# Kernel optimization log

Measured on AMD Instinct MI355X. Metric: run time of the kernel, lower is better.

## Reference

```python
import jax, jax.numpy as jnp
import numpy as np

B, LQ, LK = 4, 2048, 2048
DIM = 1024          # intermediate_dim
H, D = 16, 64       # num_heads, head_dim
AD = H * D          # attn_dim
SCALE = 1.0 / np.sqrt(D).astype(np.float32)


def setup_inputs() -> dict:
    key = jax.random.key(0)
    ks = jax.random.split(key, 12)
    init = lambda k, shape, fan_in: jax.random.normal(k, shape, jnp.float32) / np.sqrt(fan_in).astype(np.float32)
    return {
        "x": jax.random.normal(ks[0], (B, LQ, DIM), jnp.float32),
        "embeds": jax.random.normal(ks[1], (B, LK, DIM), jnp.float32),
        "Wq": init(ks[2], (DIM, AD), DIM), "bq": jnp.zeros((AD,), jnp.float32),
        "Wk": init(ks[3], (DIM, AD), DIM), "bk": jnp.zeros((AD,), jnp.float32),
        "Wv": init(ks[4], (DIM, AD), DIM), "bv": jnp.zeros((AD,), jnp.float32),
        "Wo": init(ks[5], (AD, DIM), AD), "bo": jnp.zeros((DIM,), jnp.float32),
    }


def reference(x, embeds, Wq, bq, Wk, bk, Wv, bv, Wo, bo):
    b, lq, _ = x.shape
    lk = embeds.shape[1]
    # separate QKV projections (cross-attention: K,V from embeds)
    q = (x @ Wq + bq).reshape(b, lq, H, D)
    k = (embeds @ Wk + bk).reshape(b, lk, H, D)
    v = (embeds @ Wv + bv).reshape(b, lk, H, D)
    # scaled dot-product attention; full [b,h,lq,lk] score matrix (as in source)
    scores = jnp.einsum("bqhd,bkhd->bhqk", q, k) * SCALE
    attn = jax.nn.softmax(scores, axis=-1)  # dropout is identity at eval
    ctx = jnp.einsum("bhqk,bkhd->bqhd", attn, v).reshape(b, lq, AD)
    return ctx @ Wo + bo
```

## Files before the change

kernel.cpp:

```cpp
#include <hip/hip_runtime.h>
#include <cstdint>
#include <cstddef>

#define NB   4
#define NLQ  2048
#define NLK  2048
#define NDIM 1024
#define NH   16
#define ND   64
#define NAD  1024

typedef __attribute__((ext_vector_type(8))) short bf16x8;
typedef __attribute__((ext_vector_type(4))) short sh4;
typedef __attribute__((ext_vector_type(4))) float f32x4;
typedef __attribute__((ext_vector_type(4))) int   i32x4;

static __device__ __forceinline__ short f2bf(float f) {
    unsigned u = __builtin_bit_cast(unsigned, f);
    u += 0x7fffu + ((u >> 16) & 1u);
    return (short)(u >> 16);
}

#define GLL16(GP, LP) __builtin_amdgcn_global_load_lds( \
    (const __attribute__((address_space(1))) void*)(GP), \
    (__attribute__((address_space(3))) void*)(LP), 16, 0, 0)

#define SYNC_LDS do { \
    __builtin_amdgcn_sched_barrier(0); \
    asm volatile("s_waitcnt lgkmcnt(0)" ::: "memory"); \
    __builtin_amdgcn_s_barrier(); \
    asm volatile("" ::: "memory"); \
    __builtin_amdgcn_sched_barrier(0); } while (0)

__global__ void cvt2(const float* __restrict__ x, const float* __restrict__ e,
                     short* __restrict__ xo, short* __restrict__ eo) {
    const float* in = blockIdx.y ? e : x;
    short* out = blockIdx.y ? eo : xo;
    int i = (blockIdx.x * blockDim.x + threadIdx.x) * 4;
    const float4 v = *(const float4*)(in + i);
    sh4 o;
    o.x = f2bf(v.x); o.y = f2bf(v.y); o.z = f2bf(v.z); o.w = f2bf(v.w);
    *(sh4*)(out + i) = o;
}

__global__ void wtrans4(const float* __restrict__ W0, const float* __restrict__ W1,
                        const float* __restrict__ W2, const float* __restrict__ W3,
                        short* __restrict__ T0, short* __restrict__ T1,
                        short* __restrict__ T2, short* __restrict__ T3) {
    __shared__ float t[32][33];
    const int z = blockIdx.z;
    const float* W = (z == 0) ? W0 : (z == 1) ? W1 : (z == 2) ? W2 : W3;
    short* Wt = (z == 0) ? T0 : (z == 1) ? T1 : (z == 2) ? T2 : T3;
    const int bx = blockIdx.x * 32;
    const int by = blockIdx.y * 32;
    const int tx = threadIdx.x & 31, ty = threadIdx.x >> 5;
    #pragma unroll
    for (int i = 0; i < 32; i += 8)
        t[ty + i][tx] = W[(size_t)(bx + ty + i) * 1024 + by + tx];
    __syncthreads();
    #pragma unroll
    for (int i = 0; i < 32; i += 8)
        Wt[(size_t)(by + ty + i) * 1024 + bx + tx] = f2bf(t[tx][ty + i]);
}

static __device__ __forceinline__ void xcd_tile_remap(int f, int& bx, int& by) {
    bx = ((f & 7) << 3) | ((f >> 3) & 7);
    by = f >> 6;
}


__global__ __launch_bounds__(256) void gemm_qkv(const short* __restrict__ Xb,
                                                const short* __restrict__ Eb,
                                                const short* __restrict__ Wqt,
                                                const short* __restrict__ Wkt,
                                                const short* __restrict__ Wvt,
                                                const float* __restrict__ bq,
                                                const float* __restrict__ bk,
                                                const float* __restrict__ bv,
                                                short* __restrict__ Qb,
                                                short* __restrict__ Kf,
                                                short* __restrict__ Vtb)
{
    const int N = 1024, K = 1024;
    __shared__ __align__(16) short As[128 * 64];
    __shared__ __align__(16) short Bs[128 * 64];
    const int z = blockIdx.z;
    const short* A    = (z == 0) ? Xb : Eb;
    const short* Wt   = (z == 0) ? Wqt : (z == 1) ? Wkt : Wvt;
    const float* bias = (z == 0) ? bq : (z == 1) ? bk : bv;
    const float scale = (z == 0) ? 0.18033688011112042f : 1.0f;

    const int tid = threadIdx.x, wave = tid >> 6, lane = tid & 63;
    const int quad = lane >> 4, col = lane & 15;
    int bx, by;
    xcd_tile_remap(blockIdx.x + (blockIdx.y << 6), bx, by);
    const int m0 = bx * 128, n0 = by * 128;
    const int wm = wave >> 1, wn = wave & 1;

    const f32x4 zero = {0.f, 0.f, 0.f, 0.f};
    f32x4 acc[4][4];
    #pragma unroll
    for (int i = 0; i < 4; ++i)
        #pragma unroll
        for (int j = 0; j < 4; ++j)
            acc[i][j] = zero;

    for (int kt = 0; kt < K / 64; ++kt) {
        __syncthreads();
        #pragma unroll
        for (int i = 0; i < 4; ++i) {
            const int f = (i * 4 + wave) * 512 + lane * 8;
            const int row = f >> 6, ch = (f >> 3) & 7;
            const int gcol = kt * 64 + ((ch ^ (row & 7)) * 8);
            GLL16(A  + (size_t)(m0 + row) * K + gcol, &As[f]);
            GLL16(Wt + (size_t)(n0 + row) * K + gcol, &Bs[f]);
        }
        __syncthreads();
        #pragma unroll
        for (int kk = 0; kk < 2; ++kk) {
            bf16x8 af[4], bfr[4];
            #pragma unroll
            for (int mt = 0; mt < 4; ++mt) {
                const int r = wm * 64 + mt * 16 + col;
                af[mt] = *(const bf16x8*)&As[r * 64 + (((kk * 4 + quad) ^ (r & 7)) * 8)];
            }
            #pragma unroll
            for (int nt = 0; nt < 4; ++nt) {
                const int r = wn * 64 + nt * 16 + col;
                bfr[nt] = *(const bf16x8*)&Bs[r * 64 + (((kk * 4 + quad) ^ (r & 7)) * 8)];
            }
            #pragma unroll
            for (int mt = 0; mt < 4; ++mt)
                #pragma unroll
                for (int nt = 0; nt < 4; ++nt)
                    acc[mt][nt] = __builtin_amdgcn_mfma_f32_16x16x32_bf16(af[mt], bfr[nt], acc[mt][nt], 0, 0, 0);
        }
    }

    if (z < 2) {
        short* outp = (z == 0) ? Qb : Kf;
        #pragma unroll
        for (int mt = 0; mt < 4; ++mt)
            #pragma unroll
            for (int nt = 0; nt < 4; ++nt) {
                const int n = n0 + wn * 64 + nt * 16 + col;
                const float bv_ = bias[n];
                #pragma unroll
                for (int r = 0; r < 4; ++r) {
                    const int m = m0 + wm * 64 + mt * 16 + quad * 4 + r;
                    outp[(size_t)m * N + n] = f2bf((acc[mt][nt][r] + bv_) * scale);
                }
            }
    } else {
        #pragma unroll
        for (int mt = 0; mt < 4; ++mt)
            #pragma unroll
            for (int nt = 0; nt < 4; ++nt) {
                const int n = n0 + wn * 64 + nt * 16 + col;
                const int hh = n >> 6, d = n & 63;
                const float bv_ = bias[n];
                const int mb = m0 + wm * 64 + mt * 16 + quad * 4;
                const int bb = mb >> 11, s = mb & 2047;
                sh4 o4;
                #pragma unroll
                for (int r = 0; r < 4; ++r)
                    o4[r] = f2bf(acc[mt][nt][r] + bv_);
                *(sh4*)&Vtb[((size_t)((bb * NH + hh) * 64 + d)) * NLK + s] = o4;
            }
    }
}

__global__ __launch_bounds__(256) void gemm_out(const short* __restrict__ A,
                                                const short* __restrict__ Wt,
                                                const float* __restrict__ bias,
                                                float* __restrict__ outp)
{
    const int N = 1024, K = 1024;
    __shared__ __align__(16) short As[128 * 64];
    __shared__ __align__(16) short Bs[128 * 64];
    const int tid = threadIdx.x, wave = tid >> 6, lane = tid & 63;
    const int quad = lane >> 4, col = lane & 15;
    int bx, by;
    xcd_tile_remap(blockIdx.x + (blockIdx.y << 6), bx, by);
    const int m0 = bx * 128, n0 = by * 128;
    const int wm = wave >> 1, wn = wave & 1;

    const f32x4 zero = {0.f, 0.f, 0.f, 0.f};
    f32x4 acc[4][4];
    #pragma unroll
    for (int i = 0; i < 4; ++i)
        #pragma unroll
        for (int j = 0; j < 4; ++j)
            acc[i][j] = zero;

    for (int kt = 0; kt < K / 64; ++kt) {
        __syncthreads();
        #pragma unroll
        for (int i = 0; i < 4; ++i) {
            const int f = (i * 4 + wave) * 512 + lane * 8;
            const int row = f >> 6, ch = (f >> 3) & 7;
            const int gcol = kt * 64 + ((ch ^ (row & 7)) * 8);
            GLL16(A  + (size_t)(m0 + row) * K + gcol, &As[f]);
            GLL16(Wt + (size_t)(n0 + row) * K + gcol, &Bs[f]);
        }
        __syncthreads();
        #pragma unroll
        for (int kk = 0; kk < 2; ++kk) {
            bf16x8 af[4], bfr[4];
            #pragma unroll
            for (int mt = 0; mt < 4; ++mt) {
                const int r = wm * 64 + mt * 16 + col;
                af[mt] = *(const bf16x8*)&As[r * 64 + (((kk * 4 + quad) ^ (r & 7)) * 8)];
            }
            #pragma unroll
            for (int nt = 0; nt < 4; ++nt) {
                const int r = wn * 64 + nt * 16 + col;
                bfr[nt] = *(const bf16x8*)&Bs[r * 64 + (((kk * 4 + quad) ^ (r & 7)) * 8)];
            }
            #pragma unroll
            for (int mt = 0; mt < 4; ++mt)
                #pragma unroll
                for (int nt = 0; nt < 4; ++nt)
                    acc[mt][nt] = __builtin_amdgcn_mfma_f32_16x16x32_bf16(af[mt], bfr[nt], acc[mt][nt], 0, 0, 0);
        }
    }

    #pragma unroll
    for (int mt = 0; mt < 4; ++mt)
        #pragma unroll
        for (int nt = 0; nt < 4; ++nt) {
            const int n = n0 + wn * 64 + nt * 16 + col;
            const float bv_ = bias[n];
            #pragma unroll
            for (int r = 0; r < 4; ++r) {
                const int m = m0 + wm * 64 + mt * 16 + quad * 4 + r;
                outp[(size_t)m * N + n] = acc[mt][nt][r] + bv_;
            }
        }
}

__global__ __launch_bounds__(256, 2) void attn_fused9(const short* __restrict__ Q,
                                                      const short* __restrict__ Kb,
                                                      const short* __restrict__ Vt,
                                                      short* __restrict__ ctx)
{
    __shared__ __align__(16) short Ks[2][64 * 64];
    __shared__ __align__(16) short Vs[2][64 * 64];
    const int tid = threadIdx.x, wave = tid >> 6, lane = tid & 63;
    const int quad = lane >> 4, col = lane & 15;

    const int p = blockIdx.x;
    const int g = ((p >> 3) & 7) * 8 + (p & 7);
    const int qt = p >> 6;
    const int h = g & 15, b = g >> 4;
    const int q0 = qt * 256 + wave * 64;

    bf16x8 aq[4][2];
    #pragma unroll
    for (int mt = 0; mt < 4; ++mt) {
        const short* qp = Q + (size_t)(b * NLQ + q0 + mt * 16 + col) * NAD + h * 64 + quad * 8;
        aq[mt][0] = *(const bf16x8*)qp;
        aq[mt][1] = *(const bf16x8*)(qp + 32);
    }

    bf16x8 vones;
    #pragma unroll
    for (int j = 0; j < 8; ++j) vones[j] = (short)0x3F80;

    const f32x4 zero = {0.f, 0.f, 0.f, 0.f};
    f32x4 O[4][4];
    f32x4 Ol[4];
    #pragma unroll
    for (int mt = 0; mt < 4; ++mt) {
        Ol[mt] = zero;
        #pragma unroll
        for (int db = 0; db < 4; ++db) O[db][mt] = zero;
    }

    const int srow = tid >> 3, schunk = tid & 7;
    const short* kbase = Kb + (size_t)b * NLK * NAD + h * 64 + schunk * 8;
    const short* vbase = Vt + (size_t)(b * NH + h) * 64 * NLK + schunk * 8;

    bf16x8 kv[2], vv[2];
    #pragma unroll
    for (int i = 0; i < 2; ++i) {
        const int row = i * 32 + srow;
        kv[i] = *(const bf16x8*)(kbase + (size_t)row * NAD);
        vv[i] = *(const bf16x8*)(vbase + (size_t)row * NLK);
    }

    for (int kt = 0; kt < NLK / 64; ++kt) {
        short* Kw = &Ks[kt & 1][0];
        short* Vw = &Vs[kt & 1][0];
        #pragma unroll
        for (int i = 0; i < 2; ++i) {
            const int row = i * 32 + srow;
            const int c = (schunk ^ (row & 7)) * 8;
            *(bf16x8*)&Kw[row * 64 + c] = kv[i];
            *(bf16x8*)&Vw[row * 64 + c] = vv[i];
        }

        const int nk = (kt + 1) & (NLK / 64 - 1);
        #pragma unroll
        for (int i = 0; i < 2; ++i) {
            const int row = i * 32 + srow;
            kv[i] = *(const bf16x8*)(kbase + (size_t)(nk * 64 + row) * NAD);
            vv[i] = *(const bf16x8*)(vbase + (size_t)row * NLK + nk * 64);
        }

        SYNC_LDS;

        bf16x8 kf[2][4];
        #pragma unroll
        for (int kk = 0; kk < 2; ++kk)
            #pragma unroll
            for (int nt = 0; nt < 4; ++nt) {
                const int key = nt * 16 + col;
                kf[kk][nt] = *(const bf16x8*)&Kw[key * 64 + (((kk * 4 + quad) ^ (key & 7)) * 8)];
            }

        int pk[4][2][4];
        #pragma unroll
        for (int mt = 0; mt < 4; ++mt) {
            f32x4 st[4];
            #pragma unroll
            for (int nt = 0; nt < 4; ++nt) st[nt] = zero;
            __builtin_amdgcn_s_setprio(1);
            #pragma unroll
            for (int kk = 0; kk < 2; ++kk)
                #pragma unroll
                for (int nt = 0; nt < 4; ++nt)
                    st[nt] = __builtin_amdgcn_mfma_f32_16x16x32_bf16(kf[kk][nt], aq[mt][kk], st[nt], 0, 0, 0);
            __builtin_amdgcn_s_setprio(0);
            #pragma unroll
            for (int nt = 0; nt < 4; ++nt) {
                const unsigned u0 = __builtin_bit_cast(unsigned, __builtin_amdgcn_exp2f(st[nt][0]));
                const unsigned u1 = __builtin_bit_cast(unsigned, __builtin_amdgcn_exp2f(st[nt][1]));
                const unsigned u2 = __builtin_bit_cast(unsigned, __builtin_amdgcn_exp2f(st[nt][2]));
                const unsigned u3 = __builtin_bit_cast(unsigned, __builtin_amdgcn_exp2f(st[nt][3]));
                const int t = nt >> 1, odd = (nt & 1) * 2;
                pk[mt][t][odd + 0] = (int)__builtin_amdgcn_perm(u1, u0, 0x07060302u);
                pk[mt][t][odd + 1] = (int)__builtin_amdgcn_perm(u3, u2, 0x07060302u);
            }
            __builtin_amdgcn_s_setprio(1);
            #pragma unroll
            for (int t = 0; t < 2; ++t) {
                const bf16x8 pb = __builtin_bit_cast(bf16x8,
                    i32x4{pk[mt][t][0], pk[mt][t][1], pk[mt][t][2], pk[mt][t][3]});
                Ol[mt] = __builtin_amdgcn_mfma_f32_16x16x32_bf16(vones, pb, Ol[mt], 0, 0, 0);
            }
            __builtin_amdgcn_s_setprio(0);
        }

        #pragma unroll
        for (int t = 0; t < 2; ++t)
            #pragma unroll
            for (int db = 0; db < 4; ++db) {
                const int row = db * 16 + col;
                const int c0 = t * 32 + quad * 4;
                const int c1 = t * 32 + 16 + quad * 4;
                const sh4 lo = *(const sh4*)&Vw[row * 64 + (((c0 >> 3) ^ (row & 7)) * 8 + (c0 & 7))];
                const sh4 hi = *(const sh4*)&Vw[row * 64 + (((c1 >> 3) ^ (row & 7)) * 8 + (c1 & 7))];
                bf16x8 va;
                #pragma unroll
                for (int j = 0; j < 4; ++j) { va[j] = lo[j]; va[j + 4] = hi[j]; }
                __builtin_amdgcn_s_setprio(1);
                #pragma unroll
                for (int mt = 0; mt < 4; ++mt) {
                    const bf16x8 pb = __builtin_bit_cast(bf16x8,
                        i32x4{pk[mt][t][0], pk[mt][t][1], pk[mt][t][2], pk[mt][t][3]});
                    O[db][mt] = __builtin_amdgcn_mfma_f32_16x16x32_bf16(va, pb, O[db][mt], 0, 0, 0);
                }
                __builtin_amdgcn_s_setprio(0);
            }
    }

    #pragma unroll
    for (int mt = 0; mt < 4; ++mt) {
        const float linv = 1.0f / Ol[mt][0];
        #pragma unroll
        for (int db = 0; db < 4; ++db) {
            sh4 o4;
            #pragma unroll
            for (int r = 0; r < 4; ++r)
                o4[r] = f2bf(O[db][mt][r] * linv);
            short* cp = ctx + (size_t)(b * NLQ + q0 + mt * 16 + col) * NAD
                      + h * 64 + db * 16 + quad * 4;
            *(sh4*)cp = o4;
        }
    }
}

extern "C" void kernel_launch(void* const* d_in, const int* in_sizes, int n_in,
                              void* d_out, int out_size, void* d_ws, size_t ws_size,
                              hipStream_t stream)
{
    (void)in_sizes; (void)n_in; (void)out_size; (void)ws_size;
    const float* x  = (const float*)d_in[0];
    const float* e  = (const float*)d_in[1];
    const float* Wq = (const float*)d_in[2];
    const float* bq = (const float*)d_in[3];
    const float* Wk = (const float*)d_in[4];
    const float* bk = (const float*)d_in[5];
    const float* Wv = (const float*)d_in[6];
    const float* bv = (const float*)d_in[7];
    const float* Wo = (const float*)d_in[8];
    const float* bo = (const float*)d_in[9];
    float* out = (float*)d_out;

    const size_t MQ = (size_t)NB * NLQ;
    short* wsp = (short*)d_ws;
    short* Xb  = wsp;
    short* Eb  = Xb  + MQ * NDIM;
    short* Wqt = Eb  + MQ * NDIM;
    short* Wkt = Wqt + (size_t)NDIM * NAD;
    short* Wvt = Wkt + (size_t)NDIM * NAD;
    short* Wot = Wvt + (size_t)NDIM * NAD;
    short* Qb  = Wot + (size_t)NDIM * NAD;
    short* Kf  = Qb  + MQ * NAD;
    short* Vtb = Kf  + MQ * NAD;
    short* Cx  = Vtb + MQ * NAD;

    cvt2<<<dim3(8192, 2), 256, 0, stream>>>(x, e, Xb, Eb);
    wtrans4<<<dim3(32, 32, 4), 256, 0, stream>>>(Wq, Wk, Wv, Wo, Wqt, Wkt, Wvt, Wot);

    gemm_qkv<<<dim3(64, 8, 3), 256, 0, stream>>>(Xb, Eb, Wqt, Wkt, Wvt,
                                                 bq, bk, bv, Qb, Kf, Vtb);

    attn_fused9<<<dim3(NB * NH * (NLQ / 256)), 256, 0, stream>>>(Qb, Kf, Vtb, Cx);

    gemm_out<<<dim3(64, 8), 256, 0, stream>>>(Cx, Wot, bo, out);
}
```

Measured before the change: 290.5 us.

## Software-pipeline attention: overlap previous tile's PV MFMAs with current QK/softmax

The attention loop is restructured so the P·V matmul for key tile kt-1 is interleaved with the QK^T and exp work for tile kt. It uses ping-pong P register buffers (pkA/pkB) and a 4-deep LDS ring for K/V, with a prologue and epilogue and a manually two-step unrolled loop. The aim is to hide the latency of the exp/pack dependency chain behind independent MFMAs. In exchange it raises register pressure from the doubled P buffers and doubles LDS use, which may hurt occupancy at the 2-blocks-per-CU launch bound.

```diff
diff --git a/kernel.cpp b/kernel.cpp
--- a/kernel.cpp
+++ b/kernel.cpp
@@ -239,13 +239,13 @@
         }
 }
 
-__global__ __launch_bounds__(256, 2) void attn_fused9(const short* __restrict__ Q,
-                                                      const short* __restrict__ Kb,
-                                                      const short* __restrict__ Vt,
-                                                      short* __restrict__ ctx)
+__global__ __launch_bounds__(256, 2) void attn_fused10(const short* __restrict__ Q,
+                                                       const short* __restrict__ Kb,
+                                                       const short* __restrict__ Vt,
+                                                       short* __restrict__ ctx)
 {
-    __shared__ __align__(16) short Ks[2][64 * 64];
-    __shared__ __align__(16) short Vs[2][64 * 64];
+    __shared__ __align__(16) short Ks[4][64 * 64];
+    __shared__ __align__(16) short Vs[4][64 * 64];
     const int tid = threadIdx.x, wave = tid >> 6, lane = tid & 63;
     const int quad = lane >> 4, col = lane & 15;
 
@@ -282,33 +282,33 @@
     const short* vbase = Vt + (size_t)(b * NH + h) * 64 * NLK + schunk * 8;
 
     bf16x8 kv[2], vv[2];
-    #pragma unroll
-    for (int i = 0; i < 2; ++i) {
-        const int row = i * 32 + srow;
-        kv[i] = *(const bf16x8*)(kbase + (size_t)row * NAD);
-        vv[i] = *(const bf16x8*)(vbase + (size_t)row * NLK);
-    }
-
-    for (int kt = 0; kt < NLK / 64; ++kt) {
-        short* Kw = &Ks[kt & 1][0];
-        short* Vw = &Vs[kt & 1][0];
-        #pragma unroll
-        for (int i = 0; i < 2; ++i) {
-            const int row = i * 32 + srow;
-            const int c = (schunk ^ (row & 7)) * 8;
-            *(bf16x8*)&Kw[row * 64 + c] = kv[i];
-            *(bf16x8*)&Vw[row * 64 + c] = vv[i];
-        }
-
-        const int nk = (kt + 1) & (NLK / 64 - 1);
-        #pragma unroll
-        for (int i = 0; i < 2; ++i) {
-            const int row = i * 32 + srow;
-            kv[i] = *(const bf16x8*)(kbase + (size_t)(nk * 64 + row) * NAD);
-            vv[i] = *(const bf16x8*)(vbase + (size_t)row * NLK + nk * 64);
-        }
-
+    int pkA[4][2][4], pkB[4][2][4];
+
+    auto BODY = [&](int kt, int (&rd)[4][2][4], int (&wr)[4][2][4], bool doPV) {
+        {
+            short* Kw = &Ks[kt & 3][0];
+            short* Vw = &Vs[kt & 3][0];
+            #pragma unroll
+            for (int i = 0; i < 2; ++i) {
+                const int row = i * 32 + srow;
+                const int c = (schunk ^ (row & 7)) * 8;
+                *(bf16x8*)&Kw[row * 64 + c] = kv[i];
+                *(bf16x8*)&Vw[row * 64 + c] = vv[i];
+            }
+        }
+        {
+            const int nk = (kt + 1) & 31;
+            #pragma unroll
+            for (int i = 0; i < 2; ++i) {
+                const int row = i * 32 + srow;
+                kv[i] = *(const bf16x8*)(kbase + (size_t)(nk * 64 + row) * NAD);
+                vv[i] = *(const bf16x8*)(vbase + (size_t)row * NLK + nk * 64);
+            }
+        }
         SYNC_LDS;
+
+        const short* Kw = &Ks[kt & 3][0];
+        const short* Vp = &Vs[(kt - 1) & 3][0];
 
         bf16x8 kf[2][4];
         #pragma unroll
@@ -319,9 +319,8 @@
                 kf[kk][nt] = *(const bf16x8*)&Kw[key * 64 + (((kk * 4 + quad) ^ (key & 7)) * 8)];
             }
 
-        int pk[4][2][4];
-        #pragma unroll
-        for (int mt = 0; mt < 4; ++mt) {
+        #pragma unroll
+        for (int s = 0; s < 4; ++s) {
             f32x4 st[4];
             #pragma unroll
             for (int nt = 0; nt < 4; ++nt) st[nt] = zero;
@@ -330,8 +329,31 @@
             for (int kk = 0; kk < 2; ++kk)
                 #pragma unroll
                 for (int nt = 0; nt < 4; ++nt)
-                    st[nt] = __builtin_amdgcn_mfma_f32_16x16x32_bf16(kf[kk][nt], aq[mt][kk], st[nt], 0, 0, 0);
+                    st[nt] = __builtin_amdgcn_mfma_f32_16x16x32_bf16(kf[kk][nt], aq[s][kk], st[nt], 0, 0, 0);
             __builtin_amdgcn_s_setprio(0);
+
+            if (doPV) {
+                const int row = s * 16 + col;
+                #pragma unroll
+                for (int t = 0; t < 2; ++t) {
+                    const int c0 = t * 32 + quad * 4;
+                    const int c1 = t * 32 + 16 + quad * 4;
+                    const sh4 lo = *(const sh4*)&Vp[row * 64 + (((c0 >> 3) ^ (row & 7)) * 8 + (c0 & 7))];
+                    const sh4 hi = *(const sh4*)&Vp[row * 64 + (((c1 >> 3) ^ (row & 7)) * 8 + (c1 & 7))];
+                    bf16x8 va;
+                    #pragma unroll
+                    for (int j = 0; j < 4; ++j) { va[j] = lo[j]; va[j + 4] = hi[j]; }
+                    __builtin_amdgcn_s_setprio(1);
+                    #pragma unroll
+                    for (int mt = 0; mt < 4; ++mt) {
+                        const bf16x8 pb = __builtin_bit_cast(bf16x8,
+                            i32x4{rd[mt][t][0], rd[mt][t][1], rd[mt][t][2], rd[mt][t][3]});
+                        O[s][mt] = __builtin_amdgcn_mfma_f32_16x16x32_bf16(va, pb, O[s][mt], 0, 0, 0);
+                    }
+                    __builtin_amdgcn_s_setprio(0);
+                }
+            }
+
             #pragma unroll
             for (int nt = 0; nt < 4; ++nt) {
                 const unsigned u0 = __builtin_bit_cast(unsigned, __builtin_amdgcn_exp2f(st[nt][0]));
@@ -339,19 +361,37 @@
                 const unsigned u2 = __builtin_bit_cast(unsigned, __builtin_amdgcn_exp2f(st[nt][2]));
                 const unsigned u3 = __builtin_bit_cast(unsigned, __builtin_amdgcn_exp2f(st[nt][3]));
                 const int t = nt >> 1, odd = (nt & 1) * 2;
-                pk[mt][t][odd + 0] = (int)__builtin_amdgcn_perm(u1, u0, 0x07060302u);
-                pk[mt][t][odd + 1] = (int)__builtin_amdgcn_perm(u3, u2, 0x07060302u);
+                wr[s][t][odd + 0] = (int)__builtin_amdgcn_perm(u1, u0, 0x07060302u);
+                wr[s][t][odd + 1] = (int)__builtin_amdgcn_perm(u3, u2, 0x07060302u);
             }
             __builtin_amdgcn_s_setprio(1);
             #pragma unroll
             for (int t = 0; t < 2; ++t) {
                 const bf16x8 pb = __builtin_bit_cast(bf16x8,
-                    i32x4{pk[mt][t][0], pk[mt][t][1], pk[mt][t][2], pk[mt][t][3]});
-                Ol[mt] = __builtin_amdgcn_mfma_f32_16x16x32_bf16(vones, pb, Ol[mt], 0, 0, 0);
+                    i32x4{wr[s][t][0], wr[s][t][1], wr[s][t][2], wr[s][t][3]});
+                Ol[s] = __builtin_amdgcn_mfma_f32_16x16x32_bf16(vones, pb, Ol[s], 0, 0, 0);
             }
             __builtin_amdgcn_s_setprio(0);
         }
-
+    };
+
+    #pragma unroll
+    for (int i = 0; i < 2; ++i) {
+        const int row = i * 32 + srow;
+        kv[i] = *(const bf16x8*)(kbase + (size_t)row * NAD);
+        vv[i] = *(const bf16x8*)(vbase + (size_t)row * NLK);
+    }
+
+    BODY(0, pkB, pkA, false);
+    #pragma clang loop unroll(disable)
+    for (int kt = 1; kt < 31; kt += 2) {
+        BODY(kt,     pkA, pkB, true);
+        BODY(kt + 1, pkB, pkA, true);
+    }
+    BODY(31, pkA, pkB, true);
+
+    {
+        const short* Vp = &Vs[3][0];
         #pragma unroll
         for (int t = 0; t < 2; ++t)
             #pragma unroll
@@ -359,19 +399,17 @@
                 const int row = db * 16 + col;
                 const int c0 = t * 32 + quad * 4;
                 const int c1 = t * 32 + 16 + quad * 4;
-                const sh4 lo = *(const sh4*)&Vw[row * 64 + (((c0 >> 3) ^ (row & 7)) * 8 + (c0 & 7))];
-                const sh4 hi = *(const sh4*)&Vw[row * 64 + (((c1 >> 3) ^ (row & 7)) * 8 + (c1 & 7))];
+                const sh4 lo = *(const sh4*)&Vp[row * 64 + (((c0 >> 3) ^ (row & 7)) * 8 + (c0 & 7))];
+                const sh4 hi = *(const sh4*)&Vp[row * 64 + (((c1 >> 3) ^ (row & 7)) * 8 + (c1 & 7))];
                 bf16x8 va;
                 #pragma unroll
                 for (int j = 0; j < 4; ++j) { va[j] = lo[j]; va[j + 4] = hi[j]; }
-                __builtin_amdgcn_s_setprio(1);
                 #pragma unroll
                 for (int mt = 0; mt < 4; ++mt) {
                     const bf16x8 pb = __builtin_bit_cast(bf16x8,
-                        i32x4{pk[mt][t][0], pk[mt][t][1], pk[mt][t][2], pk[mt][t][3]});
+                        i32x4{pkB[mt][t][0], pkB[mt][t][1], pkB[mt][t][2], pkB[mt][t][3]});
                     O[db][mt] = __builtin_amdgcn_mfma_f32_16x16x32_bf16(va, pb, O[db][mt], 0, 0, 0);
                 }
-                __builtin_amdgcn_s_setprio(0);
             }
     }
 
@@ -427,7 +465,7 @@
     gemm_qkv<<<dim3(64, 8, 3), 256, 0, stream>>>(Xb, Eb, Wqt, Wkt, Wvt,
                                                  bq, bk, bv, Qb, Kf, Vtb);
 
-    attn_fused9<<<dim3(NB * NH * (NLQ / 256)), 256, 0, stream>>>(Qb, Kf, Vtb, Cx);
+    attn_fused10<<<dim3(NB * NH * (NLQ / 256)), 256, 0, stream>>>(Qb, Kf, Vtb, Cx);
 
     gemm_out<<<dim3(64, 8), 256, 0, stream>>>(Cx, Wot, bo, out);
 }
```

Measured after the change: 335.8 us. +15.6%, slower.
